# Kernel optimization log

Hardware: AMD Instinct MI355X
Metric: run time of the kernel (lower is better)

Reference implementation:

```python
import jax, jax.numpy as jnp
import numpy as np

BS, LATENT, HID, MAXLEN = 128, 512, 1024, 512

def setup_inputs() -> dict:
    key = jax.random.key(0)
    ks = jax.random.split(key, 12)
    s = 1.0 / np.sqrt(HID)  # pytorch default LSTM init scale
    inp = {}
    inp["decoder_input"] = jax.random.normal(ks[0], (BS, LATENT), jnp.float32)
    inp["lengths"] = jax.random.randint(ks[1], (BS,), 0, MAXLEN)
    # bidirectional single-layer LSTM params (gate order i,f,g,o; combined bias = b_ih+b_hh)
    inp["Wih_f"] = jax.random.uniform(ks[2], (4 * HID, LATENT), jnp.float32, -s, s)
    inp["Whh_f"] = jax.random.uniform(ks[3], (4 * HID, HID), jnp.float32, -s, s)
    inp["b_f"] = jax.random.uniform(ks[4], (4 * HID,), jnp.float32, -s, s)
    inp["Wih_b"] = jax.random.uniform(ks[5], (4 * HID, LATENT), jnp.float32, -s, s)
    inp["Whh_b"] = jax.random.uniform(ks[6], (4 * HID, HID), jnp.float32, -s, s)
    inp["b_b"] = jax.random.uniform(ks[7], (4 * HID,), jnp.float32, -s, s)
    # out: Linear(hidden -> latent); fc1: Linear(2*hidden -> 1)
    inp["W_out"] = jax.random.uniform(ks[8], (LATENT, HID), jnp.float32, -s, s)
    inp["b_out"] = jax.random.uniform(ks[9], (LATENT,), jnp.float32, -s, s)
    inp["W_fc1"] = jax.random.uniform(ks[10], (1, 2 * HID), jnp.float32, -s, s)
    inp["b_fc1"] = jax.random.uniform(ks[11], (1,), jnp.float32, -s, s)
    return inp

def _lstm_cell(x, h, c, Wih, Whh, b):
    z = x @ Wih.T + h @ Whh.T + b  # (bs, 4H)
    i, f, g, o = jnp.split(z, 4, axis=-1)
    c2 = jax.nn.sigmoid(f) * c + jax.nn.sigmoid(i) * jnp.tanh(g)
    h2 = jax.nn.sigmoid(o) * jnp.tanh(c2)
    return h2, c2

def reference(decoder_input, lengths, Wih_f, Whh_f, b_f, Wih_b, Whh_b, b_b,
              W_out, b_out, W_fc1, b_fc1):
    max_len = int(jnp.max(lengths))  # static decode length
    bs = decoder_input.shape[0]
    h0 = jnp.zeros((bs, HID), decoder_input.dtype)

    def step(carry, _):
        x, hf, cf, hb, cb = carry
        # bidirectional LSTM over a length-1 sequence = two cells on same input
        hf, cf = _lstm_cell(x, hf, cf, Wih_f, Whh_f, b_f)
        hb, cb = _lstm_cell(x, hb, cb, Wih_b, Whh_b, b_b)
        out_t = jnp.concatenate([hf, hb], axis=-1)  # (bs, 2H)
        # next input = out(h_n[-1]) i.e. backward-direction hidden
        x_next = hb @ W_out.T + b_out
        return (x_next, hf, cf, hb, cb), out_t

    carry0 = (decoder_input, h0, h0, h0, h0)
    _, outs = jax.lax.scan(step, carry0, xs=None, length=max_len)  # (T, bs, 2H)
    x = jnp.transpose(outs, (1, 0, 2))  # (bs, T, 2H)
    x = jax.nn.relu(x)
    return x @ W_fc1.T + b_fc1  # (bs, T, 1)
```

## Files before the change

kernel.cpp:

```cpp
#include <hip/hip_runtime.h>
#include <math.h>

typedef unsigned short u16;
typedef __attribute__((ext_vector_type(8))) short short8;
typedef __attribute__((ext_vector_type(4))) float f32x4;

__device__ __forceinline__ float sigm(float x) { return 1.0f / (1.0f + expf(-x)); }

__device__ __forceinline__ u16 f2bf(float x) {
    union { float f; unsigned u; } v; v.f = x;
    unsigned r = v.u + 0x7fffu + ((v.u >> 16) & 1u);
    return (u16)(r >> 16);
}
__device__ __forceinline__ float bf2f(u16 h) {
    union { unsigned u; float f; } v; v.u = ((unsigned)h) << 16;
    return v.f;
}
__device__ __forceinline__ f32x4 mfma16(short8 a, short8 b, f32x4 c) {
    return __builtin_amdgcn_mfma_f32_16x16x32_bf16(a, b, c, 0, 0, 0);
}
__device__ __forceinline__ void gl_lds16(const void* g, void* l) {
    __builtin_amdgcn_global_load_lds(
        (const __attribute__((address_space(1))) unsigned int*)g,
        (__attribute__((address_space(3))) unsigned int*)l, 16, 0, 0);
}
__device__ __forceinline__ int swz(int c) { return (c ^ (c >> 2)) & 3; }

#define STAGE_W(kk, buf)                                                      \
    do {                                                                      \
        _Pragma("unroll") for (int i_ = 0; i_ < 2; ++i_)                      \
            gl_lds16(Wsrc + soff[i_] + (kk),                                  \
                     sm + (buf) * 8192 + sldsoff[i_]);                        \
    } while (0)

#define LOAD_A(kk, AH_, AL_)                                                  \
    do {                                                                      \
        _Pragma("unroll") for (int ks_ = 0; ks_ < 2; ++ks_) {                 \
            AH_[ks_] = *(const short8*)(Ah + aoff + (kk) + ks_ * 32);         \
            AL_[ks_] = *(const short8*)(Al + aoff + (kk) + ks_ * 32);         \
        }                                                                     \
    } while (0)

#define COMPUTE(buf, AH_, AL_, cix)                                           \
    do {                                                                      \
        const char* bb_ = sm + (buf) * 8192;                                  \
        _Pragma("unroll") for (int ks_ = 0; ks_ < 2; ++ks_) {                 \
            short8 bh_[2], bl_[2];                                            \
            _Pragma("unroll") for (int nt_ = 0; nt_ < 2; ++nt_) {             \
                const int col_ = nt_ * 16 + l15;                              \
                const int off_ = ks_ * 2048 + col_ * 64 + ((quad ^ swz(col_)) * 16); \
                bh_[nt_] = *(const short8*)(bb_ + off_);                      \
                bl_[nt_] = *(const short8*)(bb_ + 4096 + off_);               \
            }                                                                 \
            _Pragma("unroll") for (int nt_ = 0; nt_ < 2; ++nt_) {             \
                acc[nt_] = mfma16(AH_[ks_], bh_[nt_], acc[nt_]);              \
                acc[nt_] = mfma16(AL_[ks_], bh_[nt_], acc[nt_]);              \
                acc[nt_] = mfma16(AH_[ks_], bl_[nt_], acc[nt_]);              \
            }                                                                 \
        }                                                                     \
        if (fc1w) {                                                           \
            const int kb_ = (cix) * 64 + quad * 8;                            \
            _Pragma("unroll") for (int ks_ = 0; ks_ < 2; ++ks_) {             \
                const float* wp_ = Wfc1 + kb_ + ks_ * 32;                     \
                const f32x4 w0_ = *(const f32x4*)(wp_);                       \
                const f32x4 w1_ = *(const f32x4*)(wp_ + 4);                   \
                const short8 hv_ = AH_[ks_];                                  \
                const short8 lv_ = AL_[ks_];                                  \
                _Pragma("unroll") for (int e_ = 0; e_ < 8; ++e_) {            \
                    const float v_ = bf2f((u16)hv_[e_]) + bf2f((u16)lv_[e_]); \
                    const float wv_ = (e_ < 4) ? w0_[e_] : w1_[e_ - 4];       \
                    fsum = fmaf(fmaxf(v_, 0.0f), wv_, fsum);                  \
                }                                                             \
            }                                                                 \
        }                                                                     \
    } while (0)

__global__ __launch_bounds__(256, 2) void k_step(
    const u16* __restrict__ Ah, const u16* __restrict__ Al,
    u16* __restrict__ NAh, u16* __restrict__ NAl,
    const u16* __restrict__ WH, const u16* __restrict__ WL, int wstride,
    int koff_f, int nch_f, int koff_b, int nch_b,
    const float* __restrict__ BR, float* __restrict__ CF, float* __restrict__ CB,
    const float* __restrict__ Wfc1, const float* __restrict__ bfc1,
    float* __restrict__ out, int T, int t)
{
    __shared__ __align__(16) char sm[16384];

    const int tid = threadIdx.x, bid = blockIdx.x;
    const int w = tid >> 6, lane = tid & 63, l15 = lane & 15, quad = lane >> 4;
    const int dir = bid & 1;
    const int rest = bid >> 1;
    const int rowhalf = rest >> 7, colgrp = rest & 127;
    const int nbase = dir * 4096 + colgrp * 32;
    const int koff = dir ? koff_b : koff_f;
    const int nch  = dir ? nch_b : nch_f;
    const int r0 = rowhalf * 64 + w * 16;

    const bool fc1w = (t > 0) && (dir == 0) && (colgrp == 0);

    const int sp = w >> 1, skh = w & 1;
    const u16* Wsrc = sp ? WL : WH;
    size_t soff[2];
    int sldsoff[2];
#pragma unroll
    for (int i = 0; i < 2; ++i) {
        const int col = i * 16 + (lane >> 2);
        const int s = (lane & 3) ^ swz(col);
        soff[i] = (size_t)(nbase + col) * wstride + (size_t)(koff + skh * 32 + s * 8);
        sldsoff[i] = sp * 4096 + skh * 2048 + i * 1024;
    }

    const size_t aoff = (size_t)(r0 + l15) * 2048 + (size_t)(koff + quad * 8);

    f32x4 acc[2] = {};
    short8 ahA[2], alA[2], ahB[2], alB[2];
    float fsum = 0.0f;

    STAGE_W(0, 0);
    LOAD_A(0, ahA, alA);

    for (int c = 0; c < nch; c += 2) {
        __syncthreads();
        {
            const int k1 = (c + 1) * 64;
            STAGE_W(k1, 1);
            LOAD_A(k1, ahB, alB);
        }
        COMPUTE(0, ahA, alA, c);
        __syncthreads();
        if (c + 2 < nch) {
            const int k2 = (c + 2) * 64;
            STAGE_W(k2, 0);
            LOAD_A(k2, ahA, alA);
        }
        COMPUTE(1, ahB, alB, c + 1);
    }

    __syncthreads();

    if (fc1w) {
        float v = fsum;
        v += __shfl_xor(v, 16);
        v += __shfl_xor(v, 32);
        if (lane < 16) {
            const int m = r0 + l15;
            out[(size_t)m * T + (t - 1)] = v + bfc1[0];
        }
    }

    char* zb = sm + w * 2304;
#pragma unroll
    for (int nt = 0; nt < 2; ++nt)
#pragma unroll
        for (int r = 0; r < 4; ++r)
            *(float*)(zb + (quad * 4 + r) * 144 + (nt * 16 + l15) * 4) = acc[nt][r];
    __syncthreads();

    float* C = dir ? CB : CF;
#pragma unroll
    for (int p2 = 0; p2 < 2; ++p2) {
        const int idx = p2 * 64 + lane;
        const int ml = idx >> 3;
        const int ul = idx & 7;
        const f32x4 z = *(const f32x4*)(zb + ml * 144 + ul * 16);
        const f32x4 b4 = *(const f32x4*)(BR + nbase + ul * 4);
        const float zi = z[0] + b4[0], zf = z[1] + b4[1];
        const float zg = z[2] + b4[2], zo = z[3] + b4[3];
        const int u = colgrp * 8 + ul;
        const int m = r0 + ml;
        const size_t cidx = (size_t)m * 1024 + u;
        const float cold = C[cidx];
        const float c2 = sigm(zf) * cold + sigm(zi) * tanhf(zg);
        const float h2 = sigm(zo) * tanhf(c2);
        C[cidx] = c2;
        const size_t hidx = (size_t)m * 2048 + dir * 1024 + u;
        const u16 hh = f2bf(h2);
        NAh[hidx] = hh;
        NAl[hidx] = f2bf(h2 - bf2f(hh));
    }
}

__global__ __launch_bounds__(256) void k_tail(
    const u16* __restrict__ Ah, const u16* __restrict__ Al,
    const float* __restrict__ Wfc1, const float* __restrict__ bfc1,
    float* __restrict__ out, int T)
{
    __shared__ float red[256];
    const int m = blockIdx.x, tid = threadIdx.x;
    const size_t base = (size_t)m * 2048 + tid * 8;
    const short8 hv = *(const short8*)(Ah + base);
    const short8 lv = *(const short8*)(Al + base);
    float s = 0.0f;
#pragma unroll
    for (int e = 0; e < 8; ++e) {
        const float v = bf2f((u16)hv[e]) + bf2f((u16)lv[e]);
        s = fmaf(fmaxf(v, 0.0f), Wfc1[tid * 8 + e], s);
    }
    red[tid] = s;
    __syncthreads();
    for (int off = 128; off > 0; off >>= 1) {
        if (tid < off) red[tid] += red[tid + off];
        __syncthreads();
    }
    if (tid == 0) out[(size_t)m * T + T - 1] = red[0] + bfc1[0];
}

__global__ __launch_bounds__(256, 1) void k_fold(
    const u16* __restrict__ AH, const u16* __restrict__ AL,
    const u16* __restrict__ BH, const u16* __restrict__ BL,
    const float* __restrict__ Whh_b,
    u16* __restrict__ WH, u16* __restrict__ WL)
{
    const int tid = threadIdx.x, bid = blockIdx.x;
    const int w = tid >> 6, lane = tid & 63, l15 = lane & 15, quad = lane >> 4;
    const int bm = bid >> 4, bn = bid & 15;
    const int ar0 = bm * 64 + (w & 1) * 32;
    const int br0 = bn * 64 + (w >> 1) * 32;
    f32x4 acc[2][2] = {};
    for (int k0 = 0; k0 < 512; k0 += 32) {
        short8 a_h[2], a_l[2], b_h[2], b_l[2];
#pragma unroll
        for (int mt = 0; mt < 2; ++mt) {
            const size_t o = (size_t)(ar0 + mt * 16 + l15) * 512 + k0 + quad * 8;
            a_h[mt] = *(const short8*)(AH + o);
            a_l[mt] = *(const short8*)(AL + o);
        }
#pragma unroll
        for (int nt = 0; nt < 2; ++nt) {
            const size_t o = (size_t)(br0 + nt * 16 + l15) * 512 + k0 + quad * 8;
            b_h[nt] = *(const short8*)(BH + o);
            b_l[nt] = *(const short8*)(BL + o);
        }
#pragma unroll
        for (int mt = 0; mt < 2; ++mt)
#pragma unroll
            for (int nt = 0; nt < 2; ++nt) {
                acc[mt][nt] = mfma16(a_h[mt], b_h[nt], acc[mt][nt]);
                acc[mt][nt] = mfma16(a_l[mt], b_h[nt], acc[mt][nt]);
                acc[mt][nt] = mfma16(a_h[mt], b_l[nt], acc[mt][nt]);
            }
    }
#pragma unroll
    for (int mt = 0; mt < 2; ++mt)
#pragma unroll
        for (int nt = 0; nt < 2; ++nt)
#pragma unroll
            for (int r = 0; r < 4; ++r) {
                const int row = ar0 + mt * 16 + quad * 4 + r;
                const int j = br0 + nt * 16 + l15;
                float v = acc[mt][nt][r];
                if (row >= 4096)
                    v += Whh_b[(size_t)((row & 3) * 1024 + ((row & 4095) >> 2)) * 1024 + j];
                const size_t d = (size_t)row * 2048 + 1024 + j;
                const u16 hh = f2bf(v);
                WH[d] = hh;
                WL[d] = f2bf(v - bf2f(hh));
            }
}

__global__ __launch_bounds__(256) void k_prep(
    const float* __restrict__ dec,
    const float* __restrict__ Wih_f, const float* __restrict__ Whh_f,
    const float* __restrict__ b_f, const float* __restrict__ Wih_b,
    const float* __restrict__ b_b, const float* __restrict__ W_out,
    const float* __restrict__ b_out, const float* __restrict__ b_fc1,
    u16* __restrict__ WihH, u16* __restrict__ WihL,
    u16* __restrict__ WoTH, u16* __restrict__ WoTL,
    float* __restrict__ BR0, float* __restrict__ BR1,
    u16* __restrict__ A0h, u16* __restrict__ A0l,
    u16* __restrict__ WH, u16* __restrict__ WL,
    float* __restrict__ out, int out_size)
{
    const int t = blockIdx.x * 256 + threadIdx.x;
    if (t < 524288) {
        const int colp = t >> 6, kb = (t & 63) * 8;
        const int dir = colp >> 12, u = (colp & 4095) >> 2, g = colp & 3;
        const float* src = (dir ? Wih_b : Wih_f) + (size_t)(g * 1024 + u) * 512 + kb;
        const size_t d = (size_t)colp * 512 + kb;
#pragma unroll
        for (int j = 0; j < 8; ++j) {
            const float v = src[j];
            const u16 hh = f2bf(v);
            WihH[d + j] = hh; WihL[d + j] = f2bf(v - bf2f(hh));
        }
    } else if (t < 589824) {
        const int i = t - 524288, jc = i >> 6, lb = (i & 63) * 8;
#pragma unroll
        for (int jj = 0; jj < 8; ++jj) {
            const float v = W_out[(size_t)(lb + jj) * 1024 + jc];
            const size_t d = (size_t)jc * 512 + lb + jj;
            const u16 hh = f2bf(v);
            WoTH[d] = hh; WoTL[d] = f2bf(v - bf2f(hh));
        }
    } else if (t < 598016) {
        const int colp = t - 589824;
        const int dir = colp >> 12, u = (colp & 4095) >> 2, g = colp & 3;
        const float* Wih = dir ? Wih_b : Wih_f;
        const float s = (dir ? b_b : b_f)[g * 1024 + u];
        BR0[colp] = s;
        float dot = 0.0f;
        for (int l = 0; l < 512; ++l)
            dot += Wih[(size_t)(g * 1024 + u) * 512 + l] * b_out[l];
        BR1[colp] = s + dot;
    } else if (t < 606208) {
        const int i = t - 598016, m = i >> 6, kb = (i & 63) * 8;
#pragma unroll
        for (int j = 0; j < 8; ++j) {
            const float v = dec[(size_t)m * 512 + kb + j];
            const size_t d = (size_t)m * 2048 + kb + j;
            const u16 hh = f2bf(v);
            A0h[d] = hh; A0l[d] = f2bf(v - bf2f(hh));
        }
    } else if (t < 614400) {
        const int base = (t - 606208) * 8;
        const float b0 = b_fc1[0];
#pragma unroll
        for (int j = 0; j < 8; ++j)
            if (base + j < out_size) out[base + j] = b0;
    } else {
        const int i = t - 614400, colp = i >> 7, kb = (i & 127) * 8;
        const int u = colp >> 2, g = colp & 3;
        const float* src = Whh_f + (size_t)(g * 1024 + u) * 1024 + kb;
        const size_t d = (size_t)colp * 2048 + kb;
#pragma unroll
        for (int j = 0; j < 8; ++j) {
            const float v = src[j];
            const u16 hh = f2bf(v);
            WH[d + j] = hh; WL[d + j] = f2bf(v - bf2f(hh));
        }
    }
}

extern "C" void kernel_launch(void* const* d_in, const int* in_sizes, int n_in,
                              void* d_out, int out_size, void* d_ws, size_t ws_size,
                              hipStream_t stream) {
    const float* dec   = (const float*)d_in[0];
    const float* Wih_f = (const float*)d_in[2];
    const float* Whh_f = (const float*)d_in[3];
    const float* b_f   = (const float*)d_in[4];
    const float* Wih_b = (const float*)d_in[5];
    const float* Whh_b = (const float*)d_in[6];
    const float* b_b   = (const float*)d_in[7];
    const float* W_out = (const float*)d_in[8];
    const float* b_out = (const float*)d_in[9];
    const float* W_fc1 = (const float*)d_in[10];
    const float* b_fc1 = (const float*)d_in[11];
    float* out = (float*)d_out;

    char* ws = (char*)d_ws;
    u16* WH    = (u16*)(ws);
    u16* WL    = (u16*)(ws + 33554432);
    u16* WihH  = (u16*)(ws + 67108864);
    u16* WihL  = (u16*)(ws + 75497472);
    u16* WoTH  = (u16*)(ws + 83886080);
    u16* WoTL  = (u16*)(ws + 84934656);
    u16* A0h   = (u16*)(ws + 85983232);
    u16* A0l   = (u16*)(ws + 86507520);
    u16* A1h   = (u16*)(ws + 87031808);
    u16* A1l   = (u16*)(ws + 87556096);
    float* CF  = (float*)(ws + 88080384);
    float* CB  = (float*)(ws + 88604672);
    float* BR0 = (float*)(ws + 89128960);
    float* BR1 = (float*)(ws + 89161728);

    k_prep<<<4448, 256, 0, stream>>>(dec, Wih_f, Whh_f, b_f, Wih_b, b_b,
                                     W_out, b_out, b_fc1,
                                     WihH, WihL, WoTH, WoTL, BR0, BR1,
                                     A0h, A0l, WH, WL, out, out_size);
    k_fold<<<2048, 256, 0, stream>>>(WihH, WihL, WoTH, WoTL, Whh_b, WH, WL);
    hipMemsetAsync(CF, 0, 1048576, stream);

    const int T = out_size / 128;
    u16* Abh[2] = {A0h, A1h};
    u16* Abl[2] = {A0l, A1l};
    for (int t = 0; t < T; ++t) {
        const int in = t & 1, nx = in ^ 1;
        if (t == 0) {
            k_step<<<512, 256, 0, stream>>>(A0h, A0l, A1h, A1l,
                                            WihH, WihL, 512, 0, 8, 0, 8,
                                            BR0, CF, CB, W_fc1, b_fc1, out, T, 0);
        } else {
            k_step<<<512, 256, 0, stream>>>(Abh[in], Abl[in], Abh[nx], Abl[nx],
                                            WH, WL, 2048, 0, 32, 1024, 16,
                                            BR1, CF, CB, W_fc1, b_fc1, out, T, t);
        }
    }
    k_tail<<<128, 256, 0, stream>>>(Abh[T & 1], Abl[T & 1], W_fc1, b_fc1, out, T);
}
```

Baseline: 21.79 ms.

## Pre-pack weights and activations into MFMA fragment layout, load directly to registers

Reorders the recurrent weights, the input weights and the hidden-state buffers into a fragment-major packed layout that matches the 16x16x32 MFMA operand order. The step kernel then loads operands straight from global memory into registers with a 4-deep software prefetch, dropping the LDS staging and the barriers in the K loop. Each wave now covers 32 rows by 16 columns instead of 16 by 32, and the block-to-tile mapping is remapped. This costs extra prep work and workspace for the packed copies, and leans on L2 for operand reuse now that the weights are no longer shared through LDS.

```diff
diff --git a/kernel.cpp b/kernel.cpp
--- a/kernel.cpp
+++ b/kernel.cpp
@@ -19,57 +19,39 @@
 __device__ __forceinline__ f32x4 mfma16(short8 a, short8 b, f32x4 c) {
     return __builtin_amdgcn_mfma_f32_16x16x32_bf16(a, b, c, 0, 0, 0);
 }
-__device__ __forceinline__ void gl_lds16(const void* g, void* l) {
-    __builtin_amdgcn_global_load_lds(
-        (const __attribute__((address_space(1))) unsigned int*)g,
-        (__attribute__((address_space(3))) unsigned int*)l, 16, 0, 0);
-}
-__device__ __forceinline__ int swz(int c) { return (c ^ (c >> 2)) & 3; }
-
-#define STAGE_W(kk, buf)                                                      \
+
+
+#define LOADKG(c_, S)                                                         \
     do {                                                                      \
-        _Pragma("unroll") for (int i_ = 0; i_ < 2; ++i_)                      \
-            gl_lds16(Wsrc + soff[i_] + (kk),                                  \
-                     sm + (buf) * 8192 + sldsoff[i_]);                        \
+        const size_t ao_ = (size_t)(c_) * 4096;                               \
+        aH[S][0] = *(const short8*)(abh + ao_);                               \
+        aH[S][1] = *(const short8*)(abh + ao_ + 512);                         \
+        aL[S][0] = *(const short8*)(abl + ao_);                               \
+        aL[S][1] = *(const short8*)(abl + ao_ + 512);                         \
+        const size_t bo_ = (size_t)(c_) * 512;                                \
+        bH[S] = *(const short8*)(bbh + bo_);                                  \
+        bL[S] = *(const short8*)(bbl + bo_);                                  \
     } while (0)
 
-#define LOAD_A(kk, AH_, AL_)                                                  \
+#define COMPUTE(S, c_)                                                        \
     do {                                                                      \
-        _Pragma("unroll") for (int ks_ = 0; ks_ < 2; ++ks_) {                 \
-            AH_[ks_] = *(const short8*)(Ah + aoff + (kk) + ks_ * 32);         \
-            AL_[ks_] = *(const short8*)(Al + aoff + (kk) + ks_ * 32);         \
-        }                                                                     \
-    } while (0)
-
-#define COMPUTE(buf, AH_, AL_, cix)                                           \
-    do {                                                                      \
-        const char* bb_ = sm + (buf) * 8192;                                  \
-        _Pragma("unroll") for (int ks_ = 0; ks_ < 2; ++ks_) {                 \
-            short8 bh_[2], bl_[2];                                            \
-            _Pragma("unroll") for (int nt_ = 0; nt_ < 2; ++nt_) {             \
-                const int col_ = nt_ * 16 + l15;                              \
-                const int off_ = ks_ * 2048 + col_ * 64 + ((quad ^ swz(col_)) * 16); \
-                bh_[nt_] = *(const short8*)(bb_ + off_);                      \
-                bl_[nt_] = *(const short8*)(bb_ + 4096 + off_);               \
-            }                                                                 \
-            _Pragma("unroll") for (int nt_ = 0; nt_ < 2; ++nt_) {             \
-                acc[nt_] = mfma16(AH_[ks_], bh_[nt_], acc[nt_]);              \
-                acc[nt_] = mfma16(AL_[ks_], bh_[nt_], acc[nt_]);              \
-                acc[nt_] = mfma16(AH_[ks_], bl_[nt_], acc[nt_]);              \
-            }                                                                 \
-        }                                                                     \
+        acc0 = mfma16(aH[S][0], bH[S], acc0);                                 \
+        acc1 = mfma16(aH[S][1], bH[S], acc1);                                 \
+        acc0 = mfma16(aL[S][0], bH[S], acc0);                                 \
+        acc1 = mfma16(aL[S][1], bH[S], acc1);                                 \
+        acc0 = mfma16(aH[S][0], bL[S], acc0);                                 \
+        acc1 = mfma16(aH[S][1], bL[S], acc1);                                 \
         if (fc1w) {                                                           \
-            const int kb_ = (cix) * 64 + quad * 8;                            \
-            _Pragma("unroll") for (int ks_ = 0; ks_ < 2; ++ks_) {             \
-                const float* wp_ = Wfc1 + kb_ + ks_ * 32;                     \
-                const f32x4 w0_ = *(const f32x4*)(wp_);                       \
-                const f32x4 w1_ = *(const f32x4*)(wp_ + 4);                   \
-                const short8 hv_ = AH_[ks_];                                  \
-                const short8 lv_ = AL_[ks_];                                  \
+            const int kb_ = (akg0 + (c_)) * 32 + quad * 8;                    \
+            const f32x4 w0_ = *(const f32x4*)(Wfc1 + kb_);                    \
+            const f32x4 w1_ = *(const f32x4*)(Wfc1 + kb_ + 4);                \
+            _Pragma("unroll") for (int mt_ = 0; mt_ < 2; ++mt_) {             \
+                const short8 hv_ = aH[S][mt_];                                \
+                const short8 lv_ = aL[S][mt_];                                \
                 _Pragma("unroll") for (int e_ = 0; e_ < 8; ++e_) {            \
                     const float v_ = bf2f((u16)hv_[e_]) + bf2f((u16)lv_[e_]); \
                     const float wv_ = (e_ < 4) ? w0_[e_] : w1_[e_ - 4];       \
-                    fsum = fmaf(fmaxf(v_, 0.0f), wv_, fsum);                  \
+                    fsum[mt_] = fmaf(fmaxf(v_, 0.0f), wv_, fsum[mt_]);        \
                 }                                                             \
             }                                                                 \
         }                                                                     \
@@ -78,105 +60,98 @@
 __global__ __launch_bounds__(256, 2) void k_step(
     const u16* __restrict__ Ah, const u16* __restrict__ Al,
     u16* __restrict__ NAh, u16* __restrict__ NAl,
-    const u16* __restrict__ WH, const u16* __restrict__ WL, int wstride,
-    int koff_f, int nch_f, int koff_b, int nch_b,
+    const u16* __restrict__ BFh, const u16* __restrict__ BFl,
+    const u16* __restrict__ BBh, const u16* __restrict__ BBl,
+    int nkg_f, int nkg_b, int akg0_b,
     const float* __restrict__ BR, float* __restrict__ CF, float* __restrict__ CB,
     const float* __restrict__ Wfc1, const float* __restrict__ bfc1,
     float* __restrict__ out, int T, int t)
 {
-    __shared__ __align__(16) char sm[16384];
+    __shared__ __align__(16) char sm[9216];
 
     const int tid = threadIdx.x, bid = blockIdx.x;
     const int w = tid >> 6, lane = tid & 63, l15 = lane & 15, quad = lane >> 4;
-    const int dir = bid & 1;
-    const int rest = bid >> 1;
-    const int rowhalf = rest >> 7, colgrp = rest & 127;
-    const int nbase = dir * 4096 + colgrp * 32;
-    const int koff = dir ? koff_b : koff_f;
-    const int nch  = dir ? nch_b : nch_f;
-    const int r0 = rowhalf * 64 + w * 16;
-
-    const bool fc1w = (t > 0) && (dir == 0) && (colgrp == 0);
-
-    const int sp = w >> 1, skh = w & 1;
-    const u16* Wsrc = sp ? WL : WH;
-    size_t soff[2];
-    int sldsoff[2];
-#pragma unroll
-    for (int i = 0; i < 2; ++i) {
-        const int col = i * 16 + (lane >> 2);
-        const int s = (lane & 3) ^ swz(col);
-        soff[i] = (size_t)(nbase + col) * wstride + (size_t)(koff + skh * 32 + s * 8);
-        sldsoff[i] = sp * 4096 + skh * 2048 + i * 1024;
-    }
-
-    const size_t aoff = (size_t)(r0 + l15) * 2048 + (size_t)(koff + quad * 8);
-
-    f32x4 acc[2] = {};
-    short8 ahA[2], alA[2], ahB[2], alB[2];
-    float fsum = 0.0f;
-
-    STAGE_W(0, 0);
-    LOAD_A(0, ahA, alA);
-
-    for (int c = 0; c < nch; c += 2) {
-        __syncthreads();
-        {
-            const int k1 = (c + 1) * 64;
-            STAGE_W(k1, 1);
-            LOAD_A(k1, ahB, alB);
-        }
-        COMPUTE(0, ahA, alA, c);
-        __syncthreads();
-        if (c + 2 < nch) {
-            const int k2 = (c + 2) * 64;
-            STAGE_W(k2, 0);
-            LOAD_A(k2, ahA, alA);
-        }
-        COMPUTE(1, ahB, alB, c + 1);
-    }
-
-    __syncthreads();
+    const int rh = (bid >> 3) & 1;
+    const int id = ((bid >> 4) << 3) | (bid & 7);
+    const int dir = id & 1;
+    const int cg = id >> 1;
+    const int wr = w & 1, wc = w >> 1;
+    const int r0 = rh * 64 + wr * 32;
+    const int n16 = cg * 2 + wc;
+    const int nkg = dir ? nkg_b : nkg_f;
+    const int akg0 = dir ? akg0_b : 0;
+    const u16* Bh = dir ? BBh : BFh;
+    const u16* Bl = dir ? BBl : BFl;
+
+    const bool fc1w = (t > 0) && (dir == 0) && (cg == 0) && (wc == 0);
+
+    const int mt0 = r0 >> 4;
+    const u16* abh = Ah + (size_t)akg0 * 4096 + mt0 * 512 + lane * 8;
+    const u16* abl = Al + (size_t)akg0 * 4096 + mt0 * 512 + lane * 8;
+    const u16* bbh = Bh + (size_t)n16 * nkg * 512 + lane * 8;
+    const u16* bbl = Bl + (size_t)n16 * nkg * 512 + lane * 8;
+
+    f32x4 acc0 = {}, acc1 = {};
+    short8 aH[4][2], aL[4][2], bH[4], bL[4];
+    float fsum[2] = {0.0f, 0.0f};
+
+    LOADKG(0, 0);
+    LOADKG(1, 1);
+    LOADKG(2, 2);
+    for (int c = 0; c < nkg; c += 4) {
+        if (c + 3 < nkg) LOADKG(c + 3, 3);
+        COMPUTE(0, c);
+        if (c + 4 < nkg) LOADKG(c + 4, 0);
+        COMPUTE(1, c + 1);
+        if (c + 5 < nkg) LOADKG(c + 5, 1);
+        COMPUTE(2, c + 2);
+        if (c + 6 < nkg) LOADKG(c + 6, 2);
+        COMPUTE(3, c + 3);
+    }
 
     if (fc1w) {
-        float v = fsum;
-        v += __shfl_xor(v, 16);
-        v += __shfl_xor(v, 32);
-        if (lane < 16) {
-            const int m = r0 + l15;
-            out[(size_t)m * T + (t - 1)] = v + bfc1[0];
+#pragma unroll
+        for (int mt = 0; mt < 2; ++mt) {
+            float v = fsum[mt];
+            v += __shfl_xor(v, 16);
+            v += __shfl_xor(v, 32);
+            if (lane < 16)
+                out[(size_t)(r0 + mt * 16 + l15) * T + (t - 1)] = v + bfc1[0];
         }
     }
 
     char* zb = sm + w * 2304;
 #pragma unroll
-    for (int nt = 0; nt < 2; ++nt)
+    for (int mt = 0; mt < 2; ++mt) {
+        const f32x4 a = mt ? acc1 : acc0;
 #pragma unroll
         for (int r = 0; r < 4; ++r)
-            *(float*)(zb + (quad * 4 + r) * 144 + (nt * 16 + l15) * 4) = acc[nt][r];
-    __syncthreads();
-
+            *(float*)(zb + (mt * 16 + quad * 4 + r) * 72 + l15 * 4) = a[r];
+    }
     float* C = dir ? CB : CF;
 #pragma unroll
-    for (int p2 = 0; p2 < 2; ++p2) {
-        const int idx = p2 * 64 + lane;
-        const int ml = idx >> 3;
-        const int ul = idx & 7;
-        const f32x4 z = *(const f32x4*)(zb + ml * 144 + ul * 16);
-        const f32x4 b4 = *(const f32x4*)(BR + nbase + ul * 4);
+    for (int p = 0; p < 2; ++p) {
+        const int idx = p * 64 + lane;
+        const int ml = idx >> 2;
+        const int ul = idx & 3;
+        const f32x4 z = *(const f32x4*)(zb + ml * 72 + ul * 16);
+        const int colb = dir * 4096 + n16 * 16 + ul * 4;
+        const f32x4 b4 = *(const f32x4*)(BR + colb);
         const float zi = z[0] + b4[0], zf = z[1] + b4[1];
         const float zg = z[2] + b4[2], zo = z[3] + b4[3];
-        const int u = colgrp * 8 + ul;
+        const int u = n16 * 4 + ul;
         const int m = r0 + ml;
         const size_t cidx = (size_t)m * 1024 + u;
         const float cold = C[cidx];
         const float c2 = sigm(zf) * cold + sigm(zi) * tanhf(zg);
         const float h2 = sigm(zo) * tanhf(c2);
         C[cidx] = c2;
-        const size_t hidx = (size_t)m * 2048 + dir * 1024 + u;
+        const int kA = dir * 1024 + u;
+        const size_t ia = (size_t)(kA >> 5) * 4096 + (m >> 4) * 512
+                        + ((kA >> 3) & 3) * 128 + (m & 15) * 8 + (kA & 7);
         const u16 hh = f2bf(h2);
-        NAh[hidx] = hh;
-        NAl[hidx] = f2bf(h2 - bf2f(hh));
+        NAh[ia] = hh;
+        NAl[ia] = f2bf(h2 - bf2f(hh));
     }
 }
 
@@ -187,7 +162,8 @@
 {
     __shared__ float red[256];
     const int m = blockIdx.x, tid = threadIdx.x;
-    const size_t base = (size_t)m * 2048 + tid * 8;
+    const size_t base = (size_t)(tid >> 2) * 4096 + (m >> 4) * 512
+                      + (tid & 3) * 128 + (m & 15) * 8;
     const short8 hv = *(const short8*)(Ah + base);
     const short8 lv = *(const short8*)(Al + base);
     float s = 0.0f;
@@ -209,7 +185,8 @@
     const u16* __restrict__ AH, const u16* __restrict__ AL,
     const u16* __restrict__ BH, const u16* __restrict__ BL,
     const float* __restrict__ Whh_b,
-    u16* __restrict__ WH, u16* __restrict__ WL)
+    u16* __restrict__ PFH, u16* __restrict__ PFL,
+    u16* __restrict__ PBH, u16* __restrict__ PBL)
 {
     const int tid = threadIdx.x, bid = blockIdx.x;
     const int w = tid >> 6, lane = tid & 63, l15 = lane & 15, quad = lane >> 4;
@@ -251,10 +228,18 @@
                 float v = acc[mt][nt][r];
                 if (row >= 4096)
                     v += Whh_b[(size_t)((row & 3) * 1024 + ((row & 4095) >> 2)) * 1024 + j];
-                const size_t d = (size_t)row * 2048 + 1024 + j;
                 const u16 hh = f2bf(v);
-                WH[d] = hh;
-                WL[d] = f2bf(v - bf2f(hh));
+                const u16 ll = f2bf(v - bf2f(hh));
+                if (row < 4096) {
+                    const size_t ix = (size_t)((row >> 4) * 64 + 32 + (j >> 5)) * 512
+                                    + ((j >> 3) & 3) * 128 + (row & 15) * 8 + (j & 7);
+                    PFH[ix] = hh; PFL[ix] = ll;
+                } else {
+                    const int rl = row - 4096;
+                    const size_t ix = (size_t)((rl >> 4) * 32 + (j >> 5)) * 512
+                                    + ((j >> 3) & 3) * 128 + (rl & 15) * 8 + (j & 7);
+                    PBH[ix] = hh; PBL[ix] = ll;
+                }
             }
 }
 
@@ -268,7 +253,8 @@
     u16* __restrict__ WoTH, u16* __restrict__ WoTL,
     float* __restrict__ BR0, float* __restrict__ BR1,
     u16* __restrict__ A0h, u16* __restrict__ A0l,
-    u16* __restrict__ WH, u16* __restrict__ WL,
+    u16* __restrict__ PFH, u16* __restrict__ PFL,
+    u16* __restrict__ P0H, u16* __restrict__ P0L,
     float* __restrict__ out, int out_size)
 {
     const int t = blockIdx.x * 256 + threadIdx.x;
@@ -304,12 +290,13 @@
         BR1[colp] = s + dot;
     } else if (t < 606208) {
         const int i = t - 598016, m = i >> 6, kb = (i & 63) * 8;
+        const size_t ia = (size_t)(kb >> 5) * 4096 + (m >> 4) * 512
+                        + ((kb >> 3) & 3) * 128 + (m & 15) * 8;
 #pragma unroll
         for (int j = 0; j < 8; ++j) {
             const float v = dec[(size_t)m * 512 + kb + j];
-            const size_t d = (size_t)m * 2048 + kb + j;
-            const u16 hh = f2bf(v);
-            A0h[d] = hh; A0l[d] = f2bf(v - bf2f(hh));
+            const u16 hh = f2bf(v);
+            A0h[ia + j] = hh; A0l[ia + j] = f2bf(v - bf2f(hh));
         }
     } else if (t < 614400) {
         const int base = (t - 606208) * 8;
@@ -317,16 +304,29 @@
 #pragma unroll
         for (int j = 0; j < 8; ++j)
             if (base + j < out_size) out[base + j] = b0;
-    } else {
+    } else if (t < 1138688) {
         const int i = t - 614400, colp = i >> 7, kb = (i & 127) * 8;
         const int u = colp >> 2, g = colp & 3;
         const float* src = Whh_f + (size_t)(g * 1024 + u) * 1024 + kb;
-        const size_t d = (size_t)colp * 2048 + kb;
+        const size_t ix = (size_t)((colp >> 4) * 64 + (kb >> 5)) * 512
+                        + ((kb >> 3) & 3) * 128 + (colp & 15) * 8;
 #pragma unroll
         for (int j = 0; j < 8; ++j) {
             const float v = src[j];
             const u16 hh = f2bf(v);
-            WH[d + j] = hh; WL[d + j] = f2bf(v - bf2f(hh));
+            PFH[ix + j] = hh; PFL[ix + j] = f2bf(v - bf2f(hh));
+        }
+    } else {
+        const int i = t - 1138688, colp = i >> 6, kb = (i & 63) * 8;
+        const int dir = colp >> 12, u = (colp & 4095) >> 2, g = colp & 3;
+        const float* src = (dir ? Wih_b : Wih_f) + (size_t)(g * 1024 + u) * 512 + kb;
+        const size_t ix = (size_t)((colp >> 4) * 16 + (kb >> 5)) * 512
+                        + ((kb >> 3) & 3) * 128 + (colp & 15) * 8;
+#pragma unroll
+        for (int j = 0; j < 8; ++j) {
+            const float v = src[j];
+            const u16 hh = f2bf(v);
+            P0H[ix + j] = hh; P0L[ix + j] = f2bf(v - bf2f(hh));
         }
     }
 }
@@ -348,26 +348,31 @@
     float* out = (float*)d_out;
 
     char* ws = (char*)d_ws;
-    u16* WH    = (u16*)(ws);
-    u16* WL    = (u16*)(ws + 33554432);
-    u16* WihH  = (u16*)(ws + 67108864);
-    u16* WihL  = (u16*)(ws + 75497472);
-    u16* WoTH  = (u16*)(ws + 83886080);
-    u16* WoTL  = (u16*)(ws + 84934656);
-    u16* A0h   = (u16*)(ws + 85983232);
-    u16* A0l   = (u16*)(ws + 86507520);
-    u16* A1h   = (u16*)(ws + 87031808);
-    u16* A1l   = (u16*)(ws + 87556096);
+    u16* PFH  = (u16*)(ws);
+    u16* PFL  = (u16*)(ws + 16777216);
+    u16* PBH  = (u16*)(ws + 33554432);
+    u16* PBL  = (u16*)(ws + 41943040);
+    u16* P0H  = (u16*)(ws + 50331648);
+    u16* P0L  = (u16*)(ws + 58720256);
+    u16* WihH = (u16*)(ws + 67108864);
+    u16* WihL = (u16*)(ws + 75497472);
+    u16* WoTH = (u16*)(ws + 83886080);
+    u16* WoTL = (u16*)(ws + 84934656);
+    u16* A0h  = (u16*)(ws + 85983232);
+    u16* A0l  = (u16*)(ws + 86507520);
+    u16* A1h  = (u16*)(ws + 87031808);
+    u16* A1l  = (u16*)(ws + 87556096);
     float* CF  = (float*)(ws + 88080384);
     float* CB  = (float*)(ws + 88604672);
     float* BR0 = (float*)(ws + 89128960);
     float* BR1 = (float*)(ws + 89161728);
 
-    k_prep<<<4448, 256, 0, stream>>>(dec, Wih_f, Whh_f, b_f, Wih_b, b_b,
+    k_prep<<<6496, 256, 0, stream>>>(dec, Wih_f, Whh_f, b_f, Wih_b, b_b,
                                      W_out, b_out, b_fc1,
                                      WihH, WihL, WoTH, WoTL, BR0, BR1,
-                                     A0h, A0l, WH, WL, out, out_size);
-    k_fold<<<2048, 256, 0, stream>>>(WihH, WihL, WoTH, WoTL, Whh_b, WH, WL);
+                                     A0h, A0l, PFH, PFL, P0H, P0L, out, out_size);
+    k_fold<<<2048, 256, 0, stream>>>(WihH, WihL, WoTH, WoTL, Whh_b,
+                                     PFH, PFL, PBH, PBL);
     hipMemsetAsync(CF, 0, 1048576, stream);
 
     const int T = out_size / 128;
@@ -377,11 +382,13 @@
         const int in = t & 1, nx = in ^ 1;
         if (t == 0) {
             k_step<<<512, 256, 0, stream>>>(A0h, A0l, A1h, A1l,
-                                            WihH, WihL, 512, 0, 8, 0, 8,
+                                            P0H, P0L, P0H + 2097152, P0L + 2097152,
+                                            16, 16, 0,
                                             BR0, CF, CB, W_fc1, b_fc1, out, T, 0);
         } else {
             k_step<<<512, 256, 0, stream>>>(Abh[in], Abl[in], Abh[nx], Abl[nx],
-                                            WH, WL, 2048, 0, 32, 1024, 16,
+                                            PFH, PFL, PBH, PBL,
+                                            64, 32, 32,
                                             BR1, CF, CB, W_fc1, b_fc1, out, T, t);
         }
     }
```

Result: no change. 22.10 ms (+1.4%).
